# Kernel tuning notes

Measured on AMD Instinct MI355X. Metric: run time of the kernel, lower is better.

Reference implementation:

```python
import jax, jax.numpy as jnp
import numpy as np

N_SRC = 100_000   # hetero[s].num_nodes
N_DST = 100_000   # hetero[d].num_nodes
E     = 800_000   # edge_index.size(1)
D_SRC = 256       # node_dims['src']
D_DST = 256       # node_dims['dst']
D_REL = 128       # d_rel


def setup_inputs() -> dict:
    key = jax.random.key(0)
    ks = jax.random.split(key, 6)
    x_src = jax.random.normal(ks[0], (N_SRC, D_SRC), jnp.float32)
    x_dst = jax.random.normal(ks[1], (N_DST, D_DST), jnp.float32)
    # nn.Linear(d_in, d_rel, bias=False) weights, stored transposed as [d_in, d_rel]
    W_src = jax.random.normal(ks[2], (D_SRC, D_REL), jnp.float32) / np.sqrt(D_SRC).astype(np.float32)
    W_dst = jax.random.normal(ks[3], (D_DST, D_REL), jnp.float32) / np.sqrt(D_DST).astype(np.float32)
    edge_src = jax.random.randint(ks[4], (E,), 0, N_SRC, jnp.int32)  # edge_index[0]
    edge_dst = jax.random.randint(ks[5], (E,), 0, N_DST, jnp.int32)  # edge_index[1]
    return {"x_src": x_src, "x_dst": x_dst, "W_src": W_src, "W_dst": W_dst,
            "edge_src": edge_src, "edge_dst": edge_dst}


def reference(x_src, x_dst, W_src, W_dst, edge_src, edge_dst):
    # Per-type linear projection (bias-free), as in self.proj[nt](feats)
    p_src = x_src @ W_src            # [N_src, d_rel]
    p_dst = x_dst @ W_dst            # projected per module, unused by this edge type
    del p_dst

    # Degree of each destination (A.sum(dim=1)), clamped to >= 1.
    deg = jax.ops.segment_sum(jnp.ones((E,), jnp.float32), edge_dst,
                              num_segments=N_DST)
    deg = jnp.maximum(deg, 1.0)      # [N_dst]

    # Degree-normalized SpMM: sum of source features per destination / deg.
    # (coalescing duplicate edges sums their unit values; segment_sum matches.)
    agg = jax.ops.segment_sum(p_src[edge_src], edge_dst,
                              num_segments=N_DST)            # [N_dst, d_rel]
    dst = agg / deg[:, None]

    # rel_embs[et] = {'dst': dst, 'src_in': x_proj[s], 'deg_dst': deg}
    return dst, p_src, deg
```

## Files before the change

kernel.cpp:

```cpp
#include <hip/hip_runtime.h>
#include <hip/hip_bf16.h>

#define D_SRC 256
#define D_REL 128

typedef __bf16 bf16x8 __attribute__((ext_vector_type(8)));
typedef float f32x4 __attribute__((ext_vector_type(4)));

__global__ void zero_kernel(int* __restrict__ p, int n) {
    int i = blockIdx.x * 256 + threadIdx.x;
    if (i < n) p[i] = 0;
}

__global__ __launch_bounds__(64) void prep_w_kernel(const float* __restrict__ W,
                                                    bf16x8* __restrict__ Wt) {
    int c = blockIdx.x;
    int ks = c >> 3, n = c & 7;
    int lane = threadIdx.x;
    int col = n * 16 + (lane & 15);
    int k0 = ks * 32 + (lane >> 4) * 8;
    bf16x8 v;
#pragma unroll
    for (int j = 0; j < 8; ++j) v[j] = (__bf16)W[(size_t)(k0 + j) * D_REL + col];
    Wt[c * 64 + lane] = v;
}

__global__ __launch_bounds__(256, 4) void proj_mfma_kernel(
    const float* __restrict__ x, const bf16x8* __restrict__ Wt,
    float* __restrict__ out, unsigned short* __restrict__ out_bf, int M) {
    int tid = threadIdx.x;
    int wave = tid >> 6, lane = tid & 63;
    int row0 = blockIdx.x * 32 + (wave >> 1) * 16;
    int n0 = (wave & 1) * 4;
    int r15 = lane & 15, kb = lane >> 4;

    int rowc = min(row0 + r15, M - 1);
    const float* xr = x + (size_t)rowc * D_SRC + kb * 8;

    f32x4 a[16];
#pragma unroll
    for (int i = 0; i < 8; ++i) {
        a[2 * i + 0] = *(const f32x4*)(xr + i * 32);
        a[2 * i + 1] = *(const f32x4*)(xr + i * 32 + 4);
    }

    f32x4 acc[4];
#pragma unroll
    for (int n = 0; n < 4; ++n) acc[n] = (f32x4)(0.f);

#pragma unroll
    for (int ks = 0; ks < 8; ++ks) {
        bf16x8 b0 = Wt[(ks * 8 + n0 + 0) * 64 + lane];
        bf16x8 b1 = Wt[(ks * 8 + n0 + 1) * 64 + lane];
        bf16x8 b2 = Wt[(ks * 8 + n0 + 2) * 64 + lane];
        bf16x8 b3 = Wt[(ks * 8 + n0 + 3) * 64 + lane];
        f32x4 a0 = a[2 * ks], a1 = a[2 * ks + 1];
        bf16x8 af;
        af[0] = (__bf16)a0[0]; af[1] = (__bf16)a0[1];
        af[2] = (__bf16)a0[2]; af[3] = (__bf16)a0[3];
        af[4] = (__bf16)a1[0]; af[5] = (__bf16)a1[1];
        af[6] = (__bf16)a1[2]; af[7] = (__bf16)a1[3];
        acc[0] = __builtin_amdgcn_mfma_f32_16x16x32_bf16(af, b0, acc[0], 0, 0, 0);
        acc[1] = __builtin_amdgcn_mfma_f32_16x16x32_bf16(af, b1, acc[1], 0, 0, 0);
        acc[2] = __builtin_amdgcn_mfma_f32_16x16x32_bf16(af, b2, acc[2], 0, 0, 0);
        acc[3] = __builtin_amdgcn_mfma_f32_16x16x32_bf16(af, b3, acc[3], 0, 0, 0);
    }

    int rbase = row0 + kb * 4;
#pragma unroll
    for (int reg = 0; reg < 4; ++reg) {
        int r = rbase + reg;
        if (r < M) {
            size_t o = (size_t)r * D_REL + n0 * 16 + r15;
#pragma unroll
            for (int n = 0; n < 4; ++n) {
                float v = acc[n][reg];
                out[o + n * 16] = v;
                out_bf[o + n * 16] = __bfloat16_as_ushort(__float2bfloat16(v));
            }
        }
    }
}

__global__ void count_kernel(const int* __restrict__ edge_dst, int* __restrict__ deg_i,
                             int* __restrict__ pos_arr, int E) {
    int e = blockIdx.x * 256 + threadIdx.x;
    if (e < E) pos_arr[e] = atomicAdd(&deg_i[edge_dst[e]], 1);
}

__global__ __launch_bounds__(1024) void scan_blocks(
    const int* __restrict__ deg_i, int* __restrict__ incl,
    int* __restrict__ bsums, int n) {
    int i = blockIdx.x * 1024 + threadIdx.x;
    int v = (i < n) ? deg_i[i] : 0;
    int lane = threadIdx.x & 63;
    int wid = threadIdx.x >> 6;
    int x = v;
#pragma unroll
    for (int off = 1; off < 64; off <<= 1) {
        int y = __shfl_up(x, off, 64);
        if (lane >= off) x += y;
    }
    __shared__ int wsum[16];
    if (lane == 63) wsum[wid] = x;
    __syncthreads();
    if (wid == 0 && lane < 16) {
        int s = wsum[lane];
#pragma unroll
        for (int off = 1; off < 16; off <<= 1) {
            int y = __shfl_up(s, off, 64);
            if (lane >= off) s += y;
        }
        wsum[lane] = s;
    }
    __syncthreads();
    int add = (wid > 0) ? wsum[wid - 1] : 0;
    x += add;
    if (i < n) incl[i] = x;
    if (threadIdx.x == 1023) bsums[blockIdx.x] = x;
}

__global__ __launch_bounds__(128) void scan_sums(int* __restrict__ bs, int nb) {
    __shared__ int tmp[128];
    int t = threadIdx.x;
    int v = (t < nb) ? bs[t] : 0;
    tmp[t] = v;
    __syncthreads();
    for (int off = 1; off < 128; off <<= 1) {
        int y = 0;
        if (t >= off) y = tmp[t - off];
        __syncthreads();
        tmp[t] += y;
        __syncthreads();
    }
    if (t < nb) bs[t] = tmp[t] - v;
}

__global__ __launch_bounds__(1024) void finalize_kernel(
    const int* __restrict__ deg_i, const int* __restrict__ incl,
    const int* __restrict__ bsums, int* __restrict__ row_start,
    float* __restrict__ deg_out, int n, int E) {
    int i = blockIdx.x * 1024 + threadIdx.x;
    if (i < n) {
        int off = bsums[blockIdx.x];
        row_start[i] = off + incl[i] - deg_i[i];
        deg_out[i] = (float)max(deg_i[i], 1);
    }
    if (i == 0) row_start[n] = E;
}

__global__ void fill_kernel(const int* __restrict__ edge_src,
                            const int* __restrict__ edge_dst,
                            const int* __restrict__ row_start,
                            const int* __restrict__ pos_arr,
                            int* __restrict__ bucket, int E) {
    int e = blockIdx.x * 256 + threadIdx.x;
    if (e < E) {
        int d = edge_dst[e];
        bucket[row_start[d] + pos_arr[e]] = edge_src[e];
    }
}

__global__ __launch_bounds__(256) void gather_kernel(
    const unsigned int* __restrict__ p_bf, const int* __restrict__ row_start,
    const int* __restrict__ bucket, const float* __restrict__ deg_out,
    float* __restrict__ dst, int n) {
    int row = blockIdx.x * 4 + (threadIdx.x >> 6);
    int lane = threadIdx.x & 63;
    if (row >= n) return;
    int beg = row_start[row], end = row_start[row + 1];
    float ax = 0.f, ay = 0.f;
    int idx = beg;
    for (; idx + 4 <= end; idx += 4) {
        int s0 = bucket[idx + 0];
        int s1 = bucket[idx + 1];
        int s2 = bucket[idx + 2];
        int s3 = bucket[idx + 3];
        unsigned int v0 = p_bf[(size_t)s0 * 64 + lane];
        unsigned int v1 = p_bf[(size_t)s1 * 64 + lane];
        unsigned int v2 = p_bf[(size_t)s2 * 64 + lane];
        unsigned int v3 = p_bf[(size_t)s3 * 64 + lane];
        ax += __uint_as_float(v0 << 16) + __uint_as_float(v1 << 16)
            + __uint_as_float(v2 << 16) + __uint_as_float(v3 << 16);
        ay += __uint_as_float(v0 & 0xffff0000u) + __uint_as_float(v1 & 0xffff0000u)
            + __uint_as_float(v2 & 0xffff0000u) + __uint_as_float(v3 & 0xffff0000u);
    }
    for (; idx < end; ++idx) {
        int s = bucket[idx];
        unsigned int v = p_bf[(size_t)s * 64 + lane];
        ax += __uint_as_float(v << 16);
        ay += __uint_as_float(v & 0xffff0000u);
    }
    float dinv = 1.0f / deg_out[row];
    float2 o;
    o.x = ax * dinv;
    o.y = ay * dinv;
    ((float2*)dst)[(size_t)row * 64 + lane] = o;
}

extern "C" void kernel_launch(void* const* d_in, const int* in_sizes, int n_in,
                              void* d_out, int out_size, void* d_ws, size_t ws_size,
                              hipStream_t stream) {
    const float* x_src = (const float*)d_in[0];
    const float* W_src = (const float*)d_in[2];
    const int* edge_src = (const int*)d_in[4];
    const int* edge_dst = (const int*)d_in[5];

    const int N_SRC = in_sizes[0] / D_SRC;
    const int N_DST = in_sizes[1] / D_SRC;
    const int E = in_sizes[4];

    float* out_dst = (float*)d_out;
    float* out_psrc = out_dst + (size_t)N_DST * D_REL;
    float* out_deg = out_psrc + (size_t)N_SRC * D_REL;

    int* deg_i = (int*)d_ws;
    int* incl = deg_i + N_DST;
    int* row_start = incl + N_DST;
    int* bsums = row_start + N_DST + 1;
    int* pos_arr = bsums + 128;
    int* bucket = pos_arr + E;
    size_t int_bytes = (size_t)(3 * N_DST + 1 + 128 + 2 * (size_t)E) * sizeof(int);
    size_t wt_off = (int_bytes + 255) & ~(size_t)255;
    bf16x8* Wt = (bf16x8*)((char*)d_ws + wt_off);
    size_t pbf_off = wt_off + 65536;
    unsigned short* p_bf = (unsigned short*)((char*)d_ws + pbf_off);

    zero_kernel<<<(N_DST + 255) / 256, 256, 0, stream>>>(deg_i, N_DST);
    prep_w_kernel<<<64, 64, 0, stream>>>(W_src, Wt);
    proj_mfma_kernel<<<(N_SRC + 31) / 32, 256, 0, stream>>>(
        x_src, Wt, out_psrc, p_bf, N_SRC);
    count_kernel<<<(E + 255) / 256, 256, 0, stream>>>(edge_dst, deg_i, pos_arr, E);
    int nb = (N_DST + 1023) / 1024;
    scan_blocks<<<nb, 1024, 0, stream>>>(deg_i, incl, bsums, N_DST);
    scan_sums<<<1, 128, 0, stream>>>(bsums, nb);
    finalize_kernel<<<nb, 1024, 0, stream>>>(deg_i, incl, bsums, row_start, out_deg, N_DST, E);
    fill_kernel<<<(E + 255) / 256, 256, 0, stream>>>(edge_src, edge_dst, row_start, pos_arr, bucket, E);
    gather_kernel<<<(N_DST + 3) / 4, 256, 0, stream>>>(
        (const unsigned int*)p_bf, row_start, bucket, out_deg, out_dst, N_DST);
}
```

Measured before the change: 159.0 us.

## Restructure projection GEMM with register-resident weights and double-buffered x loads

The projection kernel now keeps each wave's 32-column slice of the bf16 weights in registers and streams 64 rows per block in 16-row, half-K chunks, prefetching the next chunk of x into a second register buffer while MFMAs run on the current one. Operands are swapped so each lane's accumulator holds four contiguous columns, which allows vectorized f32x4 and ushort4 stores instead of scalar ones. The aim is to reuse weights across more rows, overlap global loads with compute, and write outputs more efficiently. It raises register pressure, so the occupancy hint drops from 4 to 3 blocks, and the grid is halved.

Result: slower. 174.2 us (+9.6%).

```diff
diff --git a/kernel.cpp b/kernel.cpp
--- a/kernel.cpp
+++ b/kernel.cpp
@@ -25,59 +25,84 @@
     Wt[c * 64 + lane] = v;
 }
 
-__global__ __launch_bounds__(256, 4) void proj_mfma_kernel(
+__global__ __launch_bounds__(256, 3) void proj_mfma_kernel(
     const float* __restrict__ x, const bf16x8* __restrict__ Wt,
     float* __restrict__ out, unsigned short* __restrict__ out_bf, int M) {
     int tid = threadIdx.x;
-    int wave = tid >> 6, lane = tid & 63;
-    int row0 = blockIdx.x * 32 + (wave >> 1) * 16;
-    int n0 = (wave & 1) * 4;
-    int r15 = lane & 15, kb = lane >> 4;
-
-    int rowc = min(row0 + r15, M - 1);
-    const float* xr = x + (size_t)rowc * D_SRC + kb * 8;
-
-    f32x4 a[16];
-#pragma unroll
-    for (int i = 0; i < 8; ++i) {
-        a[2 * i + 0] = *(const f32x4*)(xr + i * 32);
-        a[2 * i + 1] = *(const f32x4*)(xr + i * 32 + 4);
-    }
-
-    f32x4 acc[4];
-#pragma unroll
-    for (int n = 0; n < 4; ++n) acc[n] = (f32x4)(0.f);
-
-#pragma unroll
-    for (int ks = 0; ks < 8; ++ks) {
-        bf16x8 b0 = Wt[(ks * 8 + n0 + 0) * 64 + lane];
-        bf16x8 b1 = Wt[(ks * 8 + n0 + 1) * 64 + lane];
-        bf16x8 b2 = Wt[(ks * 8 + n0 + 2) * 64 + lane];
-        bf16x8 b3 = Wt[(ks * 8 + n0 + 3) * 64 + lane];
-        f32x4 a0 = a[2 * ks], a1 = a[2 * ks + 1];
-        bf16x8 af;
-        af[0] = (__bf16)a0[0]; af[1] = (__bf16)a0[1];
-        af[2] = (__bf16)a0[2]; af[3] = (__bf16)a0[3];
-        af[4] = (__bf16)a1[0]; af[5] = (__bf16)a1[1];
-        af[6] = (__bf16)a1[2]; af[7] = (__bf16)a1[3];
-        acc[0] = __builtin_amdgcn_mfma_f32_16x16x32_bf16(af, b0, acc[0], 0, 0, 0);
-        acc[1] = __builtin_amdgcn_mfma_f32_16x16x32_bf16(af, b1, acc[1], 0, 0, 0);
-        acc[2] = __builtin_amdgcn_mfma_f32_16x16x32_bf16(af, b2, acc[2], 0, 0, 0);
-        acc[3] = __builtin_amdgcn_mfma_f32_16x16x32_bf16(af, b3, acc[3], 0, 0, 0);
-    }
-
-    int rbase = row0 + kb * 4;
-#pragma unroll
-    for (int reg = 0; reg < 4; ++reg) {
-        int r = rbase + reg;
-        if (r < M) {
-            size_t o = (size_t)r * D_REL + n0 * 16 + r15;
-#pragma unroll
-            for (int n = 0; n < 4; ++n) {
-                float v = acc[n][reg];
-                out[o + n * 16] = v;
-                out_bf[o + n * 16] = __bfloat16_as_ushort(__float2bfloat16(v));
+    int wid = tid >> 6, lane = tid & 63;
+    int col0 = wid * 32;
+    int r = lane & 15, kq = lane >> 4;
+    int row0 = blockIdx.x * 64;
+
+    bf16x8 wf[2][8];
+#pragma unroll
+    for (int s = 0; s < 2; ++s)
+#pragma unroll
+        for (int ks = 0; ks < 8; ++ks)
+            wf[s][ks] = Wt[(ks * 8 + (col0 >> 4) + s) * 64 + lane];
+
+    f32x4 lx[2][8];
+    {
+        int rowc = min(row0 + r, M - 1);
+        const float* xp = x + (size_t)rowc * D_SRC + kq * 8;
+#pragma unroll
+        for (int i = 0; i < 4; ++i) {
+            lx[0][2 * i + 0] = *(const f32x4*)(xp + i * 32);
+            lx[0][2 * i + 1] = *(const f32x4*)(xp + i * 32 + 4);
+        }
+    }
+
+    f32x4 acc0 = (f32x4)(0.f), acc1 = (f32x4)(0.f);
+
+#pragma unroll
+    for (int ht = 0; ht < 8; ++ht) {
+        const int cur = ht & 1 ? 1 : 0;
+        const int nxt = cur ^ 1;
+        if (ht < 7) {
+            int t1 = (ht + 1) >> 1, h1 = (ht + 1) & 1;
+            int rowc = min(row0 + t1 * 16 + r, M - 1);
+            const float* xp = x + (size_t)rowc * D_SRC + h1 * 128 + kq * 8;
+#pragma unroll
+            for (int i = 0; i < 4; ++i) {
+                lx[nxt][2 * i + 0] = *(const f32x4*)(xp + i * 32);
+                lx[nxt][2 * i + 1] = *(const f32x4*)(xp + i * 32 + 4);
             }
+        }
+        __builtin_amdgcn_sched_barrier(0);
+#pragma unroll
+        for (int ks = 0; ks < 4; ++ks) {
+            f32x4 a0 = lx[cur][2 * ks + 0], a1 = lx[cur][2 * ks + 1];
+            bf16x8 xf;
+            xf[0] = (__bf16)a0[0]; xf[1] = (__bf16)a0[1];
+            xf[2] = (__bf16)a0[2]; xf[3] = (__bf16)a0[3];
+            xf[4] = (__bf16)a1[0]; xf[5] = (__bf16)a1[1];
+            xf[6] = (__bf16)a1[2]; xf[7] = (__bf16)a1[3];
+            int gks = (ht & 1) * 4 + ks;
+            acc0 = __builtin_amdgcn_mfma_f32_16x16x32_bf16(wf[0][gks], xf, acc0, 0, 0, 0);
+            acc1 = __builtin_amdgcn_mfma_f32_16x16x32_bf16(wf[1][gks], xf, acc1, 0, 0, 0);
+        }
+        if (ht & 1) {
+            int t = ht >> 1;
+            int prow = row0 + t * 16 + r;
+            if (prow < M) {
+                size_t o0 = (size_t)prow * D_REL + col0 + kq * 4;
+                size_t o1 = o0 + 16;
+                *(f32x4*)(out + o0) = acc0;
+                *(f32x4*)(out + o1) = acc1;
+                ushort4 b0, b1;
+                b0.x = __bfloat16_as_ushort(__float2bfloat16(acc0[0]));
+                b0.y = __bfloat16_as_ushort(__float2bfloat16(acc0[1]));
+                b0.z = __bfloat16_as_ushort(__float2bfloat16(acc0[2]));
+                b0.w = __bfloat16_as_ushort(__float2bfloat16(acc0[3]));
+                b1.x = __bfloat16_as_ushort(__float2bfloat16(acc1[0]));
+                b1.y = __bfloat16_as_ushort(__float2bfloat16(acc1[1]));
+                b1.z = __bfloat16_as_ushort(__float2bfloat16(acc1[2]));
+                b1.w = __bfloat16_as_ushort(__float2bfloat16(acc1[3]));
+                *(ushort4*)(out_bf + o0) = b0;
+                *(ushort4*)(out_bf + o1) = b1;
+            }
+            acc0 = (f32x4)(0.f);
+            acc1 = (f32x4)(0.f);
         }
     }
 }
@@ -228,7 +253,7 @@
 
     zero_kernel<<<(N_DST + 255) / 256, 256, 0, stream>>>(deg_i, N_DST);
     prep_w_kernel<<<64, 64, 0, stream>>>(W_src, Wt);
-    proj_mfma_kernel<<<(N_SRC + 31) / 32, 256, 0, stream>>>(
+    proj_mfma_kernel<<<(N_SRC + 63) / 64, 256, 0, stream>>>(
         x_src, Wt, out_psrc, p_bf, N_SRC);
     count_kernel<<<(E + 255) / 256, 256, 0, stream>>>(edge_dst, deg_i, pos_arr, E);
     int nb = (N_DST + 1023) / 1024;
```
